# Optimization experiments

Measured on AMD Instinct MI355X. Metric: run time of the kernel, lower is better.

The kernel has to match this reference:

```python
import jax, jax.numpy as jnp
import numpy as np

B, S, D_MODEL, N_HEADS, D_K, D_V = 4, 1024, 1024, 16, 64, 64


def setup_inputs() -> dict:
    key = jax.random.key(0)
    ks = jax.random.split(key, 12)
    s = 1.0 / np.sqrt(D_MODEL)
    inp = {
        'Q': jax.random.normal(ks[0], (B, S, D_MODEL), jnp.float32),
        'K': jax.random.normal(ks[1], (B, S, D_MODEL), jnp.float32),
        'V': jax.random.normal(ks[2], (B, S, D_MODEL), jnp.float32),
        'attn_mask': jax.random.randint(ks[3], (B, S, S), 0, 2) == 1,
        'Wq': jax.random.normal(ks[4], (D_MODEL, N_HEADS * D_K), jnp.float32) * s,
        'bq': jnp.zeros((N_HEADS * D_K,), jnp.float32),
        'Wk': jax.random.normal(ks[5], (D_MODEL, N_HEADS * D_K), jnp.float32) * s,
        'bk': jnp.zeros((N_HEADS * D_K,), jnp.float32),
        'Wv': jax.random.normal(ks[6], (D_MODEL, N_HEADS * D_V), jnp.float32) * s,
        'bv': jnp.zeros((N_HEADS * D_V,), jnp.float32),
        'Wo': jax.random.normal(ks[7], (N_HEADS * D_V, D_MODEL), jnp.float32) * s,
        'bo': jnp.zeros((D_MODEL,), jnp.float32),
        'gamma': jnp.ones((D_MODEL,), jnp.float32),
        'beta': jnp.zeros((D_MODEL,), jnp.float32),
    }
    return inp


def reference(Q, K, V, attn_mask, Wq, bq, Wk, bk, Wv, bv, Wo, bo, gamma, beta):
    # QKV projections -> [B, H, S, d]
    q = (Q @ Wq + bq).reshape(B, S, N_HEADS, D_K).transpose(0, 2, 1, 3)
    k = (K @ Wk + bk).reshape(B, S, N_HEADS, D_K).transpose(0, 2, 1, 3)
    v = (V @ Wv + bv).reshape(B, S, N_HEADS, D_V).transpose(0, 2, 1, 3)
    # scaled dot-product attention with explicit mask (masked_fill with -1e9)
    scores = jnp.einsum('bhqd,bhkd->bhqk', q, k) / np.sqrt(D_K)
    scores = jnp.where(attn_mask[:, None, :, :], -1e9, scores)
    attn = jax.nn.softmax(scores, axis=-1)
    context = jnp.einsum('bhqk,bhkd->bhqd', attn, v)
    context = context.transpose(0, 2, 1, 3).reshape(B, S, N_HEADS * D_V)
    # output projection + residual + LayerNorm(d_model)
    y = context @ Wo + bo + Q
    mean = jnp.mean(y, axis=-1, keepdims=True)
    var = jnp.var(y, axis=-1, keepdims=True)
    out = (y - mean) / jnp.sqrt(var + 1e-5) * gamma + beta
    return out, attn
```

## Files before the change

kernel.cpp:

```cpp
#include <hip/hip_runtime.h>

constexpr int NB = 4;
constexpr int SQ = 1024;
constexpr int DM = 1024;
constexpr int NH = 16;
constexpr int DK = 64;

typedef __attribute__((ext_vector_type(8))) __bf16 bf16x8;
typedef __attribute__((ext_vector_type(4))) float f32x4;

#define MFMA16(a, b, c) __builtin_amdgcn_mfma_f32_16x16x32_bf16((a), (b), (c), 0, 0, 0)

__device__ __forceinline__ short f2bf(float f) {
    unsigned u = __float_as_uint(f);
    unsigned r = 0x7fffu + ((u >> 16) & 1u);
    return (short)((u + r) >> 16);
}

__device__ __forceinline__ float bf2f(short s) {
    return __uint_as_float(((unsigned)(unsigned short)s) << 16);
}

__device__ __forceinline__ int4 pack_bf16x8(float4 a, float4 b) {
    union { short s[8]; int4 v; } u;
    u.s[0] = f2bf(a.x); u.s[1] = f2bf(a.y); u.s[2] = f2bf(a.z); u.s[3] = f2bf(a.w);
    u.s[4] = f2bf(b.x); u.s[5] = f2bf(b.y); u.s[6] = f2bf(b.z); u.s[7] = f2bf(b.w);
    return u.v;
}

__global__ __launch_bounds__(256) void maskpack_kernel(
    const int* __restrict__ mask, unsigned long long* __restrict__ mpk)
{
    const int wid  = (blockIdx.x * 256 + threadIdx.x) >> 6;
    const int lane = threadIdx.x & 63;
    const int nw   = (gridDim.x * 256) >> 6;
    const int nwords = NB * SQ * SQ / 64;
    for (int w = wid; w < nwords; w += nw) {
        int v = mask[(size_t)w * 64 + lane];
        unsigned long long b = __ballot(v != 0);
        if (lane == 0) mpk[w] = b;
    }
}

__global__ __launch_bounds__(256) void wtrans_kernel(
    const float* __restrict__ W0, const float* __restrict__ W1,
    const float* __restrict__ W2, const float* __restrict__ W3,
    short* __restrict__ T0, short* __restrict__ T1,
    short* __restrict__ T2, short* __restrict__ T3)
{
    const int z = blockIdx.z;
    const float* W = (z == 0) ? W0 : (z == 1) ? W1 : (z == 2) ? W2 : W3;
    short* T       = (z == 0) ? T0 : (z == 1) ? T1 : (z == 2) ? T2 : T3;
    __shared__ float tile[32][33];
    const int n0 = blockIdx.x * 32, k0 = blockIdx.y * 32;
    const int c = threadIdx.x & 31, r0 = threadIdx.x >> 5;
#pragma unroll
    for (int i = 0; i < 4; i++) {
        int r = r0 + i * 8;
        tile[r][c] = W[(size_t)(k0 + r) * DM + n0 + c];
    }
    __syncthreads();
#pragma unroll
    for (int i = 0; i < 4; i++) {
        int r = r0 + i * 8;
        T[(size_t)(n0 + r) * DM + k0 + c] = f2bf(tile[c][r]);
    }
}

template<int MODE, bool CVTA>
__device__ __forceinline__ void gemm_core(
    const void* __restrict__ Av, const short* __restrict__ BT,
    const float* __restrict__ bias, const float* __restrict__ resid,
    short* __restrict__ obf, float* __restrict__ of)
{
    __shared__ short As[128][40];
    __shared__ short Bs[128][40];
    __shared__ short Cs[128 * 72];

    const int t = threadIdx.x;
    const int m0 = blockIdx.y * 128, n0 = blockIdx.x * 128;
    const int w = t >> 6, lane = t & 63, quad = lane >> 4, l16 = lane & 15;
    const int wm = (w & 1) * 64, wn = (w >> 1) * 64;
    const int srow = t >> 2, sseg = (t & 3) * 8;
    const float* Af = (const float*)Av;
    const short* Ab = (const short*)Av;

    const f32x4 fz = {0.f, 0.f, 0.f, 0.f};
    f32x4 acc[4][4];
#pragma unroll
    for (int i = 0; i < 4; i++)
#pragma unroll
        for (int j = 0; j < 4; j++) acc[i][j] = fz;

    auto ldA = [&](int k0, int off) -> int4 {
        if constexpr (CVTA) {
            const float* p = &Af[(size_t)(m0 + off + srow) * DM + k0 + sseg];
            float4 f0 = *(const float4*)p;
            float4 f1 = *(const float4*)(p + 4);
            return pack_bf16x8(f0, f1);
        } else {
            return *(const int4*)&Ab[(size_t)(m0 + off + srow) * DM + k0 + sseg];
        }
    };
    auto ldB = [&](int k0, int off) -> int4 {
        return *(const int4*)&BT[(size_t)(n0 + off + srow) * DM + k0 + sseg];
    };

    int4 ra0 = ldA(0, 0), ra1 = ldA(0, 64);
    int4 rb0 = ldB(0, 0), rb1 = ldB(0, 64);

    for (int k0 = 0; k0 < DM; k0 += 32) {
        __syncthreads();
        *(int4*)&As[srow][sseg] = ra0;
        *(int4*)&As[64 + srow][sseg] = ra1;
        *(int4*)&Bs[srow][sseg] = rb0;
        *(int4*)&Bs[64 + srow][sseg] = rb1;
        __syncthreads();
        if (k0 + 32 < DM) {
            ra0 = ldA(k0 + 32, 0); ra1 = ldA(k0 + 32, 64);
            rb0 = ldB(k0 + 32, 0); rb1 = ldB(k0 + 32, 64);
        }
        bf16x8 af[4], bfr[4];
#pragma unroll
        for (int mi = 0; mi < 4; mi++)
            af[mi] = *(const bf16x8*)&As[wm + mi * 16 + l16][quad * 8];
#pragma unroll
        for (int ni = 0; ni < 4; ni++)
            bfr[ni] = *(const bf16x8*)&Bs[wn + ni * 16 + l16][quad * 8];
#pragma unroll
        for (int mi = 0; mi < 4; mi++)
#pragma unroll
            for (int ni = 0; ni < 4; ni++)
                acc[mi][ni] = MFMA16(af[mi], bfr[ni], acc[mi][ni]);
    }

    if constexpr (MODE == 2) {
#pragma unroll
        for (int ni = 0; ni < 4; ni++) {
            const int col = n0 + wn + ni * 16 + l16;
            const float bb = bias[col];
#pragma unroll
            for (int mi = 0; mi < 4; mi++) {
#pragma unroll
                for (int r = 0; r < 4; r++) {
                    const int row = m0 + wm + mi * 16 + quad * 4 + r;
                    of[(size_t)row * DM + col] =
                        acc[mi][ni][r] + bb + resid[(size_t)row * DM + col];
                }
            }
        }
    } else {
        for (int hf = 0; hf < 2; hf++) {
            __syncthreads();
            if ((w >> 1) == hf) {
#pragma unroll
                for (int ni = 0; ni < 4; ni++) {
                    const int cl = ni * 16 + l16;
                    const float bb = bias[n0 + hf * 64 + cl];
#pragma unroll
                    for (int mi = 0; mi < 4; mi++)
#pragma unroll
                        for (int r = 0; r < 4; r++) {
                            const int row = wm + mi * 16 + quad * 4 + r;
                            short v = f2bf(acc[mi][ni][r] + bb);
                            if (MODE == 0) Cs[row * 72 + cl] = v;
                            else           Cs[cl * 136 + row] = v;
                        }
                }
            }
            __syncthreads();
            const int hh = (n0 >> 6) + hf;
            if (MODE == 0) {
                const int row = t >> 1, sg = (t & 1) * 32;
                const int gr = m0 + row, bi = gr >> 10, s = gr & 1023;
                const short* src = &Cs[row * 72 + sg];
                short* dst = &obf[(((size_t)(bi * NH + hh)) * SQ + s) * DK + sg];
#pragma unroll
                for (int k = 0; k < 4; k++)
                    *(int4*)&dst[k * 8] = *(const int4*)&src[k * 8];
            } else {
                const int dd = t >> 2, off = (t & 3) * 32;
                const int bi = m0 >> 10;
                const short* src = &Cs[dd * 136 + off];
                short* dst = &obf[(((size_t)(bi * NH + hh)) * DK + dd) * SQ +
                                  (m0 & 1023) + off];
#pragma unroll
                for (int k = 0; k < 4; k++)
                    *(int4*)&dst[k * 8] = *(const int4*)&src[k * 8];
            }
        }
    }
}

__global__ __launch_bounds__(256) void gemm_qkv_kernel(
    const float* __restrict__ Qin, const float* __restrict__ Kin,
    const float* __restrict__ Vin,
    const short* __restrict__ WqT, const short* __restrict__ WkT,
    const short* __restrict__ WvT,
    const float* __restrict__ bq, const float* __restrict__ bk,
    const float* __restrict__ bv,
    short* __restrict__ q_ws, short* __restrict__ k_ws,
    short* __restrict__ vt_ws)
{
    const int z = blockIdx.z;
    if (z == 0)      gemm_core<0, true>(Qin, WqT, bq, nullptr, q_ws, nullptr);
    else if (z == 1) gemm_core<0, true>(Kin, WkT, bk, nullptr, k_ws, nullptr);
    else             gemm_core<1, true>(Vin, WvT, bv, nullptr, vt_ws, nullptr);
}

__global__ __launch_bounds__(256) void gemm_out_kernel(
    const short* __restrict__ ctx, const short* __restrict__ WoT,
    const float* __restrict__ bo, const float* __restrict__ resid,
    float* __restrict__ y)
{
    gemm_core<2, false>(ctx, WoT, bo, resid, nullptr, y);
}

__global__ __launch_bounds__(256, 4) void attn_kernel(
    const short* __restrict__ q_ws, const short* __restrict__ k_ws,
    const short* __restrict__ vt_ws, const unsigned* __restrict__ mpk,
    float* __restrict__ attn, short* __restrict__ ctx)
{
    __shared__ short Ps[4][16][264];
    __shared__ float Lx[4][16];

    const int t = threadIdx.x, w = t >> 6, lane = t & 63;
    const int quad = lane >> 4, l16 = lane & 15;
    const int kh = w;
    const int wgid = blockIdx.x;
    const int bh_i = (wgid & 7) + ((wgid >> 9) << 3);
    const int qt   = (wgid >> 3) & 63;
    const int h = bh_i & 15, b = bh_i >> 4;
    const size_t bh = (size_t)b * NH + h;
    const int qrow0 = qt * 16;
    const short* qb  = q_ws + (bh * SQ + qrow0) * DK;
    const short* kb  = k_ws + bh * SQ * DK + (size_t)kh * 256 * DK;
    const short* vtb = vt_ws + bh * DK * SQ;
    const unsigned* mrow = mpk + ((size_t)b * SQ + qrow0) * 32 + kh * 8;
    float* attnb = attn + (bh * SQ + (size_t)qrow0) * SQ + kh * 256;

    const bf16x8 aq0 = *(const bf16x8*)&qb[l16 * DK + quad * 8];
    const bf16x8 aq1 = *(const bf16x8*)&qb[l16 * DK + 32 + quad * 8];
    const f32x4 fz = {0.f, 0.f, 0.f, 0.f};

    float lsum = 0.f;
    f32x4 Oacc[4] = {fz, fz, fz, fz};

    for (int ch = 0; ch < 2; ch++) {
        const uint4 mw = *(const uint4*)&mrow[l16 * 32 + ch * 4];
#pragma unroll
        for (int ks = 0; ks < 4; ks++) {
#pragma unroll
            for (int ntp = 0; ntp < 2; ntp++) {
                const int nt = ks * 2 + ntp;
                const short* kp = &kb[(size_t)(ch * 128 + nt * 16 + l16) * DK + quad * 8];
                bf16x8 k0 = *(const bf16x8*)kp;
                bf16x8 k1 = *(const bf16x8*)(kp + 32);
                f32x4 a = fz;
                a = MFMA16(k0, aq0, a);
                a = MFMA16(k1, aq1, a);
                const unsigned wd = ((const unsigned*)&mw)[nt >> 1];
                union { short s[4]; uint2 v; } pb;
#pragma unroll
                for (int r = 0; r < 4; r++) {
                    unsigned bit = (wd >> ((nt & 1) * 16 + quad * 4 + r)) & 1u;
                    float p = bit ? 0.f : __expf(a[r] * 0.125f);
                    lsum += p;
                    pb.s[r] = f2bf(p);
                }
                *(uint2*)&Ps[w][l16][ch * 128 + nt * 16 + quad * 4] = pb.v;
            }
            bf16x8 ap = *(const bf16x8*)&Ps[w][l16][ch * 128 + ks * 32 + quad * 8];
#pragma unroll
            for (int dt = 0; dt < 4; dt++) {
                bf16x8 bv = *(const bf16x8*)
                    &vtb[(size_t)(dt * 16 + l16) * SQ + kh * 256 + ch * 128 + ks * 32 + quad * 8];
                Oacc[dt] = MFMA16(ap, bv, Oacc[dt]);
            }
        }
    }

    lsum += __shfl_xor(lsum, 16, 64);
    lsum += __shfl_xor(lsum, 32, 64);
    if (lane < 16) Lx[w][lane] = lsum;
    __syncthreads();
    const float invL =
        1.f / (Lx[0][l16] + Lx[1][l16] + Lx[2][l16] + Lx[3][l16] + 1e-30f);

#pragma unroll
    for (int j = 0; j < 8; j++) {
        union { int4 v; short s[8]; } u;
        u.v = *(const int4*)&Ps[w][l16][j * 32 + quad * 8];
        float4 o0, o1;
        o0.x = bf2f(u.s[0]) * invL; o0.y = bf2f(u.s[1]) * invL;
        o0.z = bf2f(u.s[2]) * invL; o0.w = bf2f(u.s[3]) * invL;
        o1.x = bf2f(u.s[4]) * invL; o1.y = bf2f(u.s[5]) * invL;
        o1.z = bf2f(u.s[6]) * invL; o1.w = bf2f(u.s[7]) * invL;
        float* dst = &attnb[(size_t)l16 * SQ + j * 32 + quad * 8];
        *(float4*)dst = o0;
        *(float4*)(dst + 4) = o1;
    }
    __syncthreads();

    float* Oxp = (float*)&Ps[0][0][0];
    if (kh != 0) {
#pragma unroll
        for (int dt = 0; dt < 4; dt++)
#pragma unroll
            for (int r = 0; r < 4; r++)
                Oxp[((kh - 1) * 64 + lane) * 16 + dt * 4 + r] = Oacc[dt][r];
    }
    __syncthreads();
    if (kh == 0) {
        float invq[4];
#pragma unroll
        for (int r = 0; r < 4; r++) {
            const int qr = quad * 4 + r;
            invq[r] = 1.f / (Lx[0][qr] + Lx[1][qr] + Lx[2][qr] + Lx[3][qr] + 1e-30f);
        }
#pragma unroll
        for (int dt = 0; dt < 4; dt++) {
            const int col = h * DK + dt * 16 + l16;
#pragma unroll
            for (int r = 0; r < 4; r++) {
                float o = Oacc[dt][r];
#pragma unroll
                for (int kk = 0; kk < 3; kk++)
                    o += Oxp[(kk * 64 + lane) * 16 + dt * 4 + r];
                ctx[((size_t)b * SQ + qrow0 + quad * 4 + r) * DM + col] =
                    f2bf(o * invq[r]);
            }
        }
    }
}

__global__ __launch_bounds__(256) void ln_kernel(
    const float* __restrict__ y, const float* __restrict__ gamma,
    const float* __restrict__ beta, float* __restrict__ out)
{
    const int r = blockIdx.x;
    const int t = threadIdx.x;
    float4 v = *(const float4*)&y[(size_t)r * DM + t * 4];
    float s  = v.x + v.y + v.z + v.w;
    float sq = v.x * v.x + v.y * v.y + v.z * v.z + v.w * v.w;
#pragma unroll
    for (int off = 32; off > 0; off >>= 1) {
        s  += __shfl_xor(s, off, 64);
        sq += __shfl_xor(sq, off, 64);
    }
    __shared__ float rs[4], rq[4];
    const int lane = t & 63, w = t >> 6;
    if (lane == 0) { rs[w] = s; rq[w] = sq; }
    __syncthreads();
    s  = rs[0] + rs[1] + rs[2] + rs[3];
    sq = rq[0] + rq[1] + rq[2] + rq[3];
    const float mean = s * (1.f / 1024.f);
    const float var  = sq * (1.f / 1024.f) - mean * mean;
    const float rstd = rsqrtf(var + 1e-5f);
    float4 g  = *(const float4*)&gamma[t * 4];
    float4 be = *(const float4*)&beta[t * 4];
    float4 o;
    o.x = (v.x - mean) * rstd * g.x + be.x;
    o.y = (v.y - mean) * rstd * g.y + be.y;
    o.z = (v.z - mean) * rstd * g.z + be.z;
    o.w = (v.w - mean) * rstd * g.w + be.w;
    *(float4*)&out[(size_t)r * DM + t * 4] = o;
}

extern "C" void kernel_launch(void* const* d_in, const int* in_sizes, int n_in,
                              void* d_out, int out_size, void* d_ws, size_t ws_size,
                              hipStream_t stream)
{
    const float* Q     = (const float*)d_in[0];
    const float* Kin   = (const float*)d_in[1];
    const float* Vin   = (const float*)d_in[2];
    const int*   mask  = (const int*)d_in[3];
    const float* Wq    = (const float*)d_in[4];
    const float* bq    = (const float*)d_in[5];
    const float* Wk    = (const float*)d_in[6];
    const float* bk    = (const float*)d_in[7];
    const float* Wv    = (const float*)d_in[8];
    const float* bv    = (const float*)d_in[9];
    const float* Wo    = (const float*)d_in[10];
    const float* bo    = (const float*)d_in[11];
    const float* gamma = (const float*)d_in[12];
    const float* beta  = (const float*)d_in[13];

    float* out  = (float*)d_out;
    float* attn = out + (size_t)NB * SQ * DM;

    const size_t NE = (size_t)NB * SQ * DM;
    const size_t WE = (size_t)DM * DM;
    short* wsb   = (short*)d_ws;
    short* WqT   = wsb;
    short* WkT   = WqT + WE;
    short* WvT   = WkT + WE;
    short* WoT   = WvT + WE;
    short* q_ws  = WoT + WE;
    short* k_ws  = q_ws + NE;
    short* vt_ws = k_ws + NE;
    short* ctx   = vt_ws + NE;
    unsigned* mpk = (unsigned*)(ctx + NE);
    float* y = (float*)q_ws;

    maskpack_kernel<<<dim3(256), 256, 0, stream>>>(
        mask, (unsigned long long*)mpk);
    wtrans_kernel<<<dim3(32, 32, 4), 256, 0, stream>>>(
        Wq, Wk, Wv, Wo, WqT, WkT, WvT, WoT);

    gemm_qkv_kernel<<<dim3(8, 32, 3), 256, 0, stream>>>(
        Q, Kin, Vin, WqT, WkT, WvT, bq, bk, bv, q_ws, k_ws, vt_ws);

    attn_kernel<<<dim3(4096), 256, 0, stream>>>(
        q_ws, k_ws, vt_ws, mpk, attn, ctx);

    gemm_out_kernel<<<dim3(8, 32, 1), 256, 0, stream>>>(ctx, WoT, bo, Q, y);

    ln_kernel<<<NB * SQ, 256, 0, stream>>>(y, gamma, beta, out);
}
```

Measured before the change: 617.7 us.

## Software-pipeline QK and PV in attention, keep P in registers, shrink LDS

The attention kernel's two nested loops become one fully unrolled 8-step loop over 32-key groups. Each step issues the PV MFMAs of the previous group while computing scores for the current one, using a double-buffered small LDS tile for P. The unnormalized probabilities are also kept in registers (pw) for the final attn write instead of being re-read from a full 256-column LDS buffer. The partial-O exchange gets its own LDS array, which removes one __syncthreads. LDS use drops, which may raise occupancy, but holding P values and the full unroll raises register pressure.

After: 615.2 us. About the same (-0.4%).

```diff
diff --git a/kernel.cpp b/kernel.cpp
--- a/kernel.cpp
+++ b/kernel.cpp
@@ -221,8 +221,9 @@
     const short* __restrict__ vt_ws, const unsigned* __restrict__ mpk,
     float* __restrict__ attn, short* __restrict__ ctx)
 {
-    __shared__ short Ps[4][16][264];
+    __shared__ short Ps[4][2][16][48];
     __shared__ float Lx[4][16];
+    __shared__ float Oxp[3][64][16];
 
     const int t = threadIdx.x, w = t >> 6, lane = t & 63;
     const int quad = lane >> 4, l16 = lane & 15;
@@ -243,42 +244,49 @@
     const bf16x8 aq1 = *(const bf16x8*)&qb[l16 * DK + 32 + quad * 8];
     const f32x4 fz = {0.f, 0.f, 0.f, 0.f};
 
+    const uint4 mwA = *(const uint4*)&mrow[l16 * 32];
+    const uint4 mwB = *(const uint4*)&mrow[l16 * 32 + 4];
+
     float lsum = 0.f;
     f32x4 Oacc[4] = {fz, fz, fz, fz};
-
-    for (int ch = 0; ch < 2; ch++) {
-        const uint4 mw = *(const uint4*)&mrow[l16 * 32 + ch * 4];
-#pragma unroll
-        for (int ks = 0; ks < 4; ks++) {
-#pragma unroll
-            for (int ntp = 0; ntp < 2; ntp++) {
-                const int nt = ks * 2 + ntp;
-                const short* kp = &kb[(size_t)(ch * 128 + nt * 16 + l16) * DK + quad * 8];
-                bf16x8 k0 = *(const bf16x8*)kp;
-                bf16x8 k1 = *(const bf16x8*)(kp + 32);
-                f32x4 a = fz;
-                a = MFMA16(k0, aq0, a);
-                a = MFMA16(k1, aq1, a);
-                const unsigned wd = ((const unsigned*)&mw)[nt >> 1];
-                union { short s[4]; uint2 v; } pb;
-#pragma unroll
-                for (int r = 0; r < 4; r++) {
-                    unsigned bit = (wd >> ((nt & 1) * 16 + quad * 4 + r)) & 1u;
-                    float p = bit ? 0.f : __expf(a[r] * 0.125f);
-                    lsum += p;
-                    pb.s[r] = f2bf(p);
-                }
-                *(uint2*)&Ps[w][l16][ch * 128 + nt * 16 + quad * 4] = pb.v;
+    uint2 pw[8][2];
+
+    auto PV = [&](int gp) {
+        bf16x8 ap = *(const bf16x8*)&Ps[w][gp & 1][l16][quad * 8];
+#pragma unroll
+        for (int dt = 0; dt < 4; dt++) {
+            bf16x8 bv = *(const bf16x8*)
+                &vtb[(size_t)(dt * 16 + l16) * SQ + kh * 256 + gp * 32 + quad * 8];
+            Oacc[dt] = MFMA16(ap, bv, Oacc[dt]);
+        }
+    };
+
+#pragma unroll
+    for (int g = 0; g < 8; g++) {
+        if (g > 0) PV(g - 1);
+        const unsigned wd = (g < 4) ? ((const unsigned*)&mwA)[g]
+                                    : ((const unsigned*)&mwB)[g - 4];
+#pragma unroll
+        for (int ntp = 0; ntp < 2; ntp++) {
+            const short* kp = &kb[(size_t)(g * 32 + ntp * 16 + l16) * DK + quad * 8];
+            bf16x8 k0 = *(const bf16x8*)kp;
+            bf16x8 k1 = *(const bf16x8*)(kp + 32);
+            f32x4 a = fz;
+            a = MFMA16(k0, aq0, a);
+            a = MFMA16(k1, aq1, a);
+            union { short s[4]; uint2 v; } pb;
+#pragma unroll
+            for (int r = 0; r < 4; r++) {
+                unsigned bit = (wd >> (ntp * 16 + quad * 4 + r)) & 1u;
+                float p = bit ? 0.f : __expf(a[r] * 0.125f);
+                lsum += p;
+                pb.s[r] = f2bf(p);
             }
-            bf16x8 ap = *(const bf16x8*)&Ps[w][l16][ch * 128 + ks * 32 + quad * 8];
-#pragma unroll
-            for (int dt = 0; dt < 4; dt++) {
-                bf16x8 bv = *(const bf16x8*)
-                    &vtb[(size_t)(dt * 16 + l16) * SQ + kh * 256 + ch * 128 + ks * 32 + quad * 8];
-                Oacc[dt] = MFMA16(ap, bv, Oacc[dt]);
-            }
-        }
-    }
+            pw[g][ntp] = pb.v;
+            *(uint2*)&Ps[w][g & 1][l16][ntp * 16 + quad * 4] = pb.v;
+        }
+    }
+    PV(7);
 
     lsum += __shfl_xor(lsum, 16, 64);
     lsum += __shfl_xor(lsum, 32, 64);
@@ -288,27 +296,25 @@
         1.f / (Lx[0][l16] + Lx[1][l16] + Lx[2][l16] + Lx[3][l16] + 1e-30f);
 
 #pragma unroll
-    for (int j = 0; j < 8; j++) {
-        union { int4 v; short s[8]; } u;
-        u.v = *(const int4*)&Ps[w][l16][j * 32 + quad * 8];
-        float4 o0, o1;
-        o0.x = bf2f(u.s[0]) * invL; o0.y = bf2f(u.s[1]) * invL;
-        o0.z = bf2f(u.s[2]) * invL; o0.w = bf2f(u.s[3]) * invL;
-        o1.x = bf2f(u.s[4]) * invL; o1.y = bf2f(u.s[5]) * invL;
-        o1.z = bf2f(u.s[6]) * invL; o1.w = bf2f(u.s[7]) * invL;
-        float* dst = &attnb[(size_t)l16 * SQ + j * 32 + quad * 8];
-        *(float4*)dst = o0;
-        *(float4*)(dst + 4) = o1;
-    }
-    __syncthreads();
-
-    float* Oxp = (float*)&Ps[0][0][0];
+    for (int g = 0; g < 8; g++) {
+#pragma unroll
+        for (int ntp = 0; ntp < 2; ntp++) {
+            const uint2 v = pw[g][ntp];
+            float4 o;
+            o.x = bf2f((short)(v.x & 0xffffu)) * invL;
+            o.y = bf2f((short)(v.x >> 16)) * invL;
+            o.z = bf2f((short)(v.y & 0xffffu)) * invL;
+            o.w = bf2f((short)(v.y >> 16)) * invL;
+            *(float4*)&attnb[(size_t)l16 * SQ + g * 32 + ntp * 16 + quad * 4] = o;
+        }
+    }
+
     if (kh != 0) {
 #pragma unroll
         for (int dt = 0; dt < 4; dt++)
 #pragma unroll
             for (int r = 0; r < 4; r++)
-                Oxp[((kh - 1) * 64 + lane) * 16 + dt * 4 + r] = Oacc[dt][r];
+                Oxp[kh - 1][lane][dt * 4 + r] = Oacc[dt][r];
     }
     __syncthreads();
     if (kh == 0) {
@@ -326,7 +332,7 @@
                 float o = Oacc[dt][r];
 #pragma unroll
                 for (int kk = 0; kk < 3; kk++)
-                    o += Oxp[(kk * 64 + lane) * 16 + dt * 4 + r];
+                    o += Oxp[kk][lane][dt * 4 + r];
                 ctx[((size_t)b * SQ + qrow0 + quad * 4 + r) * DM + col] =
                     f2bf(o * invq[r]);
             }
```
